# Optimization experiments

Hardware: AMD Instinct MI355X
Metric: run time of the kernel (lower is better)

## Reference

```python
import jax, jax.numpy as jnp
import numpy as np

D_MODEL = 768
N_HEADS = 12
D_HEAD = 64
N_MEM = 3072
ALPHA = 0.1
EPS = 1e-5
W_SCALE = 0.02  # standard init scale so energies/grads stay well-conditioned


def setup_inputs() -> dict:
    key = jax.random.key(0)
    k0, k1, k2, k3 = jax.random.split(key, 4)
    B, S = 8, 1024
    x = jax.random.normal(k0, (B, S, D_MODEL), jnp.float32)
    gamma = jnp.ones((1,), jnp.float32)                      # scalar LN gamma (ET uses a single gamma)
    delta = jnp.zeros((D_MODEL,), jnp.float32)               # LN bias
    Wq = jax.random.normal(k1, (N_HEADS, D_HEAD, D_MODEL), jnp.float32) * W_SCALE
    Wk = jax.random.normal(k2, (N_HEADS, D_HEAD, D_MODEL), jnp.float32) * W_SCALE
    beta = jnp.ones((N_HEADS,), jnp.float32) / np.sqrt(D_HEAD)  # per-head beta init 1/sqrt(d_head)
    xi = jax.random.normal(k3, (N_MEM, D_MODEL), jnp.float32) * W_SCALE
    return {"x": x, "gamma": gamma, "delta": delta, "Wq": Wq, "Wk": Wk,
            "beta": beta, "xi": xi, "n_steps": 12}


def _total_energy(x, gamma, delta, Wq, Wk, beta, xi):
    # --- EnergyLayerNorm: g = dL/dx, E_ln = <x, g> - L ---
    mean = jnp.mean(x, axis=-1, keepdims=True)
    xm = x - mean
    var = jnp.mean(xm * xm, axis=-1, keepdims=True)
    std = jnp.sqrt(var + EPS)
    g = gamma * xm / std + delta                       # (B,S,D)
    L = jnp.sum(D_MODEL * gamma * std) + jnp.sum(delta * x)
    e_ln = jnp.sum(x * g) - L
    # --- EnergyAttention: E = -sum_{b,h,q} (1/beta_h) * logsumexp_k(beta_h * Q.K) ---
    q = jnp.einsum('bsd,hyd->bhsy', g, Wq)
    k = jnp.einsum('bsd,hyd->bhsy', g, Wk)
    A = jnp.einsum('bhqy,bhky->bhqk', q, k)            # (B,H,S,S)
    lse = jax.nn.logsumexp(beta[None, :, None, None] * A, axis=-1)  # (B,H,S)
    e_attn = -jnp.sum(lse / beta[None, :, None])
    # --- HopfieldNetwork: E = -1/2 sum relu(g @ xi^T)^2 ---
    h = jnp.einsum('bsd,md->bsm', g, xi)               # (B,S,M)
    e_hop = -0.5 * jnp.sum(jnp.square(jax.nn.relu(h)))
    return e_ln + e_attn + e_hop


def reference(x, gamma, delta, Wq, Wk, beta, xi, n_steps):
    grad_fn = jax.grad(_total_energy, argnums=0)

    def step(state, _):
        return state - ALPHA * grad_fn(state, gamma, delta, Wq, Wk, beta, xi), None

    final, _ = jax.lax.scan(step, x, None, length=n_steps)
    return final
```

## Files before the change

kernel.cpp:

```cpp
#include <hip/hip_runtime.h>
#include <hip/hip_bf16.h>
#include <stdint.h>

#define T_TOK 8192
#define DM    768
#define NH    12
#define DH    64
#define SEQ   1024
#define NBH   96
#define NMEM  3072
#define NUP   4608
#define ALPHA 0.1f
#define EPS   1e-5f
#define NSTEPS 12
#define PAD   72
#define SPLITK 4

typedef unsigned short us;
typedef __bf16 bf16x8 __attribute__((ext_vector_type(8)));
typedef float  f32x4  __attribute__((ext_vector_type(4)));

__device__ __forceinline__ us f2bf(float f) {
  uint32_t u = __builtin_bit_cast(uint32_t, f);
  u += 0x7fffu + ((u >> 16) & 1u);
  return (us)(u >> 16);
}

__device__ __forceinline__ f32x4 mfma16(bf16x8 a, bf16x8 b, f32x4 c) {
  return __builtin_amdgcn_mfma_f32_16x16x32_bf16(a, b, c, 0, 0, 0);
}

__device__ __forceinline__ void gld16(const void* g, void* l) {
  __builtin_amdgcn_global_load_lds(
      (const __attribute__((address_space(1))) void*)(uintptr_t)g,
      (__attribute__((address_space(3))) void*)(uint32_t)(uintptr_t)l,
      16, 0, 0);
}

__device__ __forceinline__ float block_sum(float v, float* sb, int tid) {
#pragma unroll
  for (int d = 32; d >= 1; d >>= 1) v += __shfl_xor(v, d);
  __syncthreads();
  if ((tid & 63) == 0) sb[tid >> 6] = v;
  __syncthreads();
  return sb[0] + sb[1] + sb[2] + sb[3];
}

__global__ __launch_bounds__(256) void pack_w(const float* __restrict__ Wq,
                                              const float* __restrict__ Wk,
                                              const float* __restrict__ xi,
                                              us* __restrict__ Wup, us* __restrict__ WdT) {
  int idx = blockIdx.x * 256 + threadIdx.x;
  if (idx >= NUP * DM) return;
  int r = idx / DM, d = idx - r * DM;
  float v = (r < 768) ? Wq[idx] : (r < 1536 ? Wk[idx - 768 * DM] : xi[idx - 1536 * DM]);
  us h = f2bf(v);
  Wup[idx] = h;
  WdT[(size_t)d * NUP + r] = h;
}

__global__ __launch_bounds__(256) void ln_fwd(const float* __restrict__ X,
                                              const float* __restrict__ gamma,
                                              const float* __restrict__ delta,
                                              us* __restrict__ g_bf,
                                              float* __restrict__ meanb, float* __restrict__ rstdb) {
  int t = blockIdx.x, tid = threadIdx.x;
  const float* x = X + (size_t)t * DM;
  __shared__ float sb[4];
  float v0 = x[tid], v1 = x[tid + 256], v2 = x[tid + 512];
  float mean = block_sum(v0 + v1 + v2, sb, tid) * (1.0f / DM);
  float d0 = v0 - mean, d1 = v1 - mean, d2 = v2 - mean;
  float var = block_sum(d0 * d0 + d1 * d1 + d2 * d2, sb, tid) * (1.0f / DM);
  float rstd = rsqrtf(var + EPS);
  float gm = gamma[0];
  us* go = g_bf + (size_t)t * DM;
  go[tid]       = f2bf(gm * d0 * rstd + delta[tid]);
  go[tid + 256] = f2bf(gm * d1 * rstd + delta[tid + 256]);
  go[tid + 512] = f2bf(gm * d2 * rstd + delta[tid + 512]);
  if (tid == 0) { meanb[t] = mean; rstdb[t] = rstd; }
}

template <int MODE>
__global__ __launch_bounds__(256, 3) void gemm_bt(const us* __restrict__ A, const us* __restrict__ B,
                                                  int Kstride, int kchunk, us* __restrict__ QKout,
                                                  us* __restrict__ Dout, float* __restrict__ Gout) {
  __shared__ us As[3 * 128 * 32];
  __shared__ us Bs[3 * 128 * 32];
  int tid = threadIdx.x;
  int w = tid >> 6, lane = tid & 63, lm = lane & 15, lq = lane >> 4;
  int wm = (w >> 1) * 64, wn = (w & 1) * 64;

  int nwg  = gridDim.x * gridDim.y;
  int id   = blockIdx.y * gridDim.x + blockIdx.x;
  int qq   = nwg >> 3, rr = nwg & 7;
  int xcd  = id & 7, rank = id >> 3;
  int nid  = (xcd < rr ? xcd * (qq + 1) : rr * (qq + 1) + (xcd - rr) * qq) + rank;
  int bm   = nid % gridDim.x, bn = nid / gridDim.x;
  int m0 = bm * 128, n0 = bn * 128;
  int kbeg = blockIdx.z * kchunk;
  int NT = kchunk >> 5;

  int sr  = tid >> 2;
  int k8s = (tid & 3) ^ ((tid >> 3) & 3);
  const us* pa = A + (size_t)(m0 + sr) * Kstride + kbeg + k8s * 8;
  const us* pb = B + (size_t)(n0 + sr) * Kstride + kbeg + k8s * 8;
  const size_t hstep = (size_t)64 * Kstride;
  us* dA0 = &As[tid * 8];
  us* dB0 = &Bs[tid * 8];

  int kx   = (lq ^ ((lm >> 1) & 3)) * 8;
  int aoff = (wm + lm) * 32 + kx;
  int boff = (wn + lm) * 32 + kx;
  const us* Ar = As + aoff;
  const us* Br = Bs + boff;

  f32x4 zero4 = {0.f, 0.f, 0.f, 0.f};
  f32x4 acc[4][4];
#pragma unroll
  for (int i = 0; i < 4; i++)
#pragma unroll
    for (int j = 0; j < 4; j++) acc[i][j] = zero4;

#define STAGE_A(S, T) { gld16(pa + (size_t)(T) * 32,         dA0 + (S) * 4096); \
                        gld16(pa + (size_t)(T) * 32 + hstep, dA0 + (S) * 4096 + 2048); }
#define STAGE_B(S, T) { gld16(pb + (size_t)(T) * 32,         dB0 + (S) * 4096); \
                        gld16(pb + (size_t)(T) * 32 + hstep, dB0 + (S) * 4096 + 2048); }

  STAGE_A(0, 0); STAGE_B(0, 0);
  STAGE_A(1, 1); STAGE_B(1, 1);
  asm volatile("s_waitcnt vmcnt(4)" ::: "memory");
  __builtin_amdgcn_s_barrier();

#define ITER(T, S) {                                                            \
    bf16x8 af_[4], bf_[4];                                                      \
    _Pragma("unroll") for (int x = 0; x < 4; x++)                               \
      af_[x] = *(const bf16x8*)(Ar + (S) * 4096 + x * 512);                     \
    _Pragma("unroll") for (int x = 0; x < 4; x++)                               \
      bf_[x] = *(const bf16x8*)(Br + (S) * 4096 + x * 512);                     \
    if ((T) + 2 < NT) { STAGE_A(((S) + 2) % 3, (T) + 2);                        \
                        STAGE_B(((S) + 2) % 3, (T) + 2); }                      \
    _Pragma("unroll") for (int mt = 0; mt < 4; mt++)                            \
      _Pragma("unroll") for (int nt = 0; nt < 4; nt++)                          \
        acc[mt][nt] = mfma16(af_[mt], bf_[nt], acc[mt][nt]);                    \
    asm volatile("s_waitcnt lgkmcnt(0)" ::: "memory");                          \
    if ((T) + 2 < NT)      { asm volatile("s_waitcnt vmcnt(4)" ::: "memory"); } \
    else if ((T) + 1 < NT) { asm volatile("s_waitcnt vmcnt(0)" ::: "memory"); } \
    __builtin_amdgcn_s_barrier();                                               \
  }

  for (int t = 0; t < NT; t += 3) {
    ITER(t,     0);
    ITER(t + 1, 1);
    ITER(t + 2, 2);
  }
#undef ITER
#undef STAGE_A
#undef STAGE_B

  if (MODE == 0 && n0 < 1536) {
#pragma unroll
    for (int mt = 0; mt < 4; mt++) {
      int row = m0 + wm + mt * 16 + lq * 4;
#pragma unroll
      for (int nt = 0; nt < 4; nt++) {
        int col = n0 + wn + nt * 16 + lm;
#pragma unroll
        for (int r = 0; r < 4; r++)
          QKout[(size_t)(row + r) * 1536 + col] = f2bf(acc[mt][nt][r]);
      }
    }
  } else if (MODE == 0) {
#pragma unroll
    for (int mt = 0; mt < 4; mt++) {
      int row = m0 + wm + mt * 16 + lq * 4;
#pragma unroll
      for (int nt = 0; nt < 4; nt++) {
        int col = n0 + wn + nt * 16 + lm;
#pragma unroll
        for (int r = 0; r < 4; r++)
          Dout[(size_t)(row + r) * NUP + col] = f2bf(fmaxf(acc[mt][nt][r], 0.f));
      }
    }
  } else {
    float* Gz = Gout + (size_t)blockIdx.z * T_TOK * DM;
#pragma unroll
    for (int mt = 0; mt < 4; mt++) {
      int row = m0 + wm + mt * 16 + lq * 4;
#pragma unroll
      for (int nt = 0; nt < 4; nt++) {
        int col = n0 + wn + nt * 16 + lm;
#pragma unroll
        for (int r = 0; r < 4; r++)
          Gz[(size_t)(row + r) * DM + col] = acc[mt][nt][r];
      }
    }
  }
}

__global__ __launch_bounds__(256) void transpose_qk(const us* __restrict__ QK,
                                                    us* __restrict__ Qt, us* __restrict__ Kt) {
  int bh = blockIdx.x, kt = blockIdx.y, which = blockIdx.z;
  int b = bh / NH, h = bh - b * NH;
  int tid = threadIdx.x;
  __shared__ us tile[64][72];
  int c0 = h * 64 + (which ? 768 : 0);
  us* dst = (which ? Kt : Qt) + (size_t)bh * 64 * 1024;
#pragma unroll
  for (int r = 0; r < 2; r++) {
    int key = r * 32 + (tid >> 3); int yb = (tid & 7) * 8;
    *(bf16x8*)&tile[key][yb] =
        *(const bf16x8*)&QK[(size_t)(b * SEQ + kt * 64 + key) * 1536 + c0 + yb];
  }
  __syncthreads();
#pragma unroll
  for (int r = 0; r < 2; r++) {
    int lin = r * 256 + tid; int y = lin >> 3; int kb = (lin & 7) * 8;
    __align__(16) us tmp[8];
#pragma unroll
    for (int j = 0; j < 8; j++) tmp[j] = tile[kb + j][y];
    *(bf16x8*)&dst[(size_t)y * 1024 + kt * 64 + kb] = *(bf16x8*)tmp;
  }
}

__global__ __launch_bounds__(256) void attn_fwd(const us* __restrict__ QK, const us* __restrict__ Ktg,
                                                const float* __restrict__ beta,
                                                us* __restrict__ Dbuf, float* __restrict__ lse) {
  __shared__ us Qs[64 * PAD];
  __shared__ us Ks[64 * PAD];
  __shared__ us Kts[64 * PAD];
  __shared__ us Ps[4 * 16 * PAD];
  int bh = blockIdx.x, qt = blockIdx.y;
  int b = bh / NH, h = bh - b * NH;
  int tid = threadIdx.x, w = tid >> 6, lane = tid & 63, lm = lane & 15, lq = lane >> 4;
  float betah = beta[h];
#pragma unroll
  for (int r = 0; r < 2; r++) {
    int row = r * 32 + (tid >> 3); int yb = (tid & 7) * 8;
    *(bf16x8*)&Qs[row * PAD + yb] =
        *(const bf16x8*)&QK[(size_t)(b * SEQ + qt * 64 + row) * 1536 + h * 64 + yb];
  }
  __syncthreads();
  bf16x8 aq0 = *(const bf16x8*)&Qs[(w * 16 + lm) * PAD + lq * 8];
  bf16x8 aq1 = *(const bf16x8*)&Qs[(w * 16 + lm) * PAD + 32 + lq * 8];
  f32x4 zero = {0.f, 0.f, 0.f, 0.f};
  f32x4 O[4] = {zero, zero, zero, zero};
  float lacc[4] = {0.f, 0.f, 0.f, 0.f};
  us* pw = &Ps[w * 16 * PAD];

  for (int kc = 0; kc < SEQ; kc += 64) {
    __syncthreads();
#pragma unroll
    for (int r = 0; r < 2; r++) {
      int row = r * 32 + (tid >> 3); int yb = (tid & 7) * 8;
      *(bf16x8*)&Ks[row * PAD + yb] =
          *(const bf16x8*)&QK[(size_t)(b * SEQ + kc + row) * 1536 + 768 + h * 64 + yb];
      int lin = r * 256 + tid; int y = lin >> 3; int kb = (lin & 7) * 8;
      *(bf16x8*)&Kts[y * PAD + kb] =
          *(const bf16x8*)&Ktg[(size_t)(bh * 64 + y) * 1024 + kc + kb];
    }
    __syncthreads();
#pragma unroll
    for (int kk = 0; kk < 4; kk++) {
      f32x4 s = mfma16(aq0, *(const bf16x8*)&Ks[(kk * 16 + lm) * PAD + lq * 8], zero);
      s = mfma16(aq1, *(const bf16x8*)&Ks[(kk * 16 + lm) * PAD + 32 + lq * 8], s);
#pragma unroll
      for (int r = 0; r < 4; r++) {
        float p = __expf(betah * s[r]);
        lacc[r] += p;
        pw[(lq * 4 + r) * PAD + kk * 16 + lm] = f2bf(p);
      }
    }
    bf16x8 pa0 = *(const bf16x8*)&pw[lm * PAD + lq * 8];
    bf16x8 pa1 = *(const bf16x8*)&pw[lm * PAD + 32 + lq * 8];
#pragma unroll
    for (int nt = 0; nt < 4; nt++) {
      O[nt] = mfma16(pa0, *(const bf16x8*)&Kts[(nt * 16 + lm) * PAD + lq * 8], O[nt]);
      O[nt] = mfma16(pa1, *(const bf16x8*)&Kts[(nt * 16 + lm) * PAD + 32 + lq * 8], O[nt]);
    }
  }
  float l[4];
#pragma unroll
  for (int r = 0; r < 4; r++) {
    float v = lacc[r];
    v += __shfl_xor(v, 1); v += __shfl_xor(v, 2);
    v += __shfl_xor(v, 4); v += __shfl_xor(v, 8);
    l[r] = v;
  }
  float inv[4];
#pragma unroll
  for (int r = 0; r < 4; r++) inv[r] = 1.f / l[r];
#pragma unroll
  for (int nt = 0; nt < 4; nt++)
#pragma unroll
    for (int r = 0; r < 4; r++) {
      int q = qt * 64 + w * 16 + lq * 4 + r;
      Dbuf[(size_t)(b * SEQ + q) * NUP + h * 64 + nt * 16 + lm] = f2bf(O[nt][r] * inv[r]);
    }
  if (lm == 0) {
#pragma unroll
    for (int r = 0; r < 4; r++)
      lse[bh * SEQ + qt * 64 + w * 16 + lq * 4 + r] = __logf(l[r]);
  }
}

__global__ __launch_bounds__(256) void attn_bwd(const us* __restrict__ QK, const us* __restrict__ Qtg,
                                                const float* __restrict__ lse,
                                                const float* __restrict__ beta,
                                                us* __restrict__ Dbuf) {
  __shared__ us Ks2[64 * PAD];
  __shared__ us Qs2[64 * PAD];
  __shared__ us Qts[64 * PAD];
  __shared__ us Ps[4 * 16 * PAD];
  int bh = blockIdx.x, kt = blockIdx.y;
  int b = bh / NH, h = bh - b * NH;
  int tid = threadIdx.x, w = tid >> 6, lane = tid & 63, lm = lane & 15, lq = lane >> 4;
  float betah = beta[h];
#pragma unroll
  for (int r = 0; r < 2; r++) {
    int row = r * 32 + (tid >> 3); int yb = (tid & 7) * 8;
    *(bf16x8*)&Ks2[row * PAD + yb] =
        *(const bf16x8*)&QK[(size_t)(b * SEQ + kt * 64 + row) * 1536 + 768 + h * 64 + yb];
  }
  __syncthreads();
  bf16x8 ak0 = *(const bf16x8*)&Ks2[(w * 16 + lm) * PAD + lq * 8];
  bf16x8 ak1 = *(const bf16x8*)&Ks2[(w * 16 + lm) * PAD + 32 + lq * 8];
  f32x4 zero = {0.f, 0.f, 0.f, 0.f};
  f32x4 O[4] = {zero, zero, zero, zero};
  us* pw = &Ps[w * 16 * PAD];

  for (int qc = 0; qc < SEQ; qc += 64) {
    __syncthreads();
#pragma unroll
    for (int r = 0; r < 2; r++) {
      int row = r * 32 + (tid >> 3); int yb = (tid & 7) * 8;
      *(bf16x8*)&Qs2[row * PAD + yb] =
          *(const bf16x8*)&QK[(size_t)(b * SEQ + qc + row) * 1536 + h * 64 + yb];
      int lin = r * 256 + tid; int y = lin >> 3; int qb = (lin & 7) * 8;
      *(bf16x8*)&Qts[y * PAD + qb] =
          *(const bf16x8*)&Qtg[(size_t)(bh * 64 + y) * 1024 + qc + qb];
    }
    __syncthreads();
#pragma unroll
    for (int kk = 0; kk < 4; kk++) {
      f32x4 s = mfma16(ak0, *(const bf16x8*)&Qs2[(kk * 16 + lm) * PAD + lq * 8], zero);
      s = mfma16(ak1, *(const bf16x8*)&Qs2[(kk * 16 + lm) * PAD + 32 + lq * 8], s);
      float lv = lse[bh * SEQ + qc + kk * 16 + lm];
#pragma unroll
      for (int r = 0; r < 4; r++)
        pw[(lq * 4 + r) * PAD + kk * 16 + lm] = f2bf(__expf(betah * s[r] - lv));
    }
    bf16x8 pa0 = *(const bf16x8*)&pw[lm * PAD + lq * 8];
    bf16x8 pa1 = *(const bf16x8*)&pw[lm * PAD + 32 + lq * 8];
#pragma unroll
    for (int nt = 0; nt < 4; nt++) {
      O[nt] = mfma16(pa0, *(const bf16x8*)&Qts[(nt * 16 + lm) * PAD + lq * 8], O[nt]);
      O[nt] = mfma16(pa1, *(const bf16x8*)&Qts[(nt * 16 + lm) * PAD + 32 + lq * 8], O[nt]);
    }
  }
#pragma unroll
  for (int nt = 0; nt < 4; nt++)
#pragma unroll
    for (int r = 0; r < 4; r++) {
      int key = kt * 64 + w * 16 + lq * 4 + r;
      Dbuf[(size_t)(b * SEQ + key) * NUP + 768 + h * 64 + nt * 16 + lm] = f2bf(O[nt][r]);
    }
}

__global__ __launch_bounds__(256) void update_x(float* __restrict__ X, const float* __restrict__ G,
                                                float* __restrict__ meanb,
                                                float* __restrict__ rstdb,
                                                const float* __restrict__ gamma,
                                                const float* __restrict__ delta,
                                                us* __restrict__ g_bf) {
  int t = blockIdx.x, tid = threadIdx.x;
  __shared__ float sb[4];
  float mean = meanb[t], rstd = rstdb[t], gm = gamma[0];
  float* x = X + (size_t)t * DM;
  const float* g0 = G + (size_t)t * DM;
  const size_t GS = (size_t)T_TOK * DM;
  int i0 = tid, i1 = tid + 256, i2 = tid + 512;
  float x0 = x[i0], x1 = x[i1], x2 = x[i2];
  float gv0 = 0.f, gv1 = 0.f, gv2 = 0.f;
#pragma unroll
  for (int z = 0; z < SPLITK; z++) {
    gv0 += g0[i0 + z * GS];
    gv1 += g0[i1 + z * GS];
    gv2 += g0[i2 + z * GS];
  }
  float v0 = x0 - gv0, v1 = x1 - gv1, v2 = x2 - gv2;
  float n0 = (x0 - mean) * rstd, n1 = (x1 - mean) * rstd, n2 = (x2 - mean) * rstd;
  float s1 = block_sum(v0 + v1 + v2, sb, tid) * (1.0f / DM);
  float s2 = block_sum(v0 * n0 + v1 * n1 + v2 * n2, sb, tid) * (1.0f / DM);
  float c = ALPHA * gm * rstd;
  float y0 = x0 - c * (v0 - s1 - n0 * s2);
  float y1 = x1 - c * (v1 - s1 - n1 * s2);
  float y2 = x2 - c * (v2 - s1 - n2 * s2);
  x[i0] = y0; x[i1] = y1; x[i2] = y2;
  float mean2 = block_sum(y0 + y1 + y2, sb, tid) * (1.0f / DM);
  float d0 = y0 - mean2, d1 = y1 - mean2, d2 = y2 - mean2;
  float var2 = block_sum(d0 * d0 + d1 * d1 + d2 * d2, sb, tid) * (1.0f / DM);
  float rstd2 = rsqrtf(var2 + EPS);
  us* go = g_bf + (size_t)t * DM;
  go[i0] = f2bf(gm * d0 * rstd2 + delta[i0]);
  go[i1] = f2bf(gm * d1 * rstd2 + delta[i1]);
  go[i2] = f2bf(gm * d2 * rstd2 + delta[i2]);
  if (tid == 0) { meanb[t] = mean2; rstdb[t] = rstd2; }
}

extern "C" void kernel_launch(void* const* d_in, const int* in_sizes, int n_in,
                              void* d_out, int out_size, void* d_ws, size_t ws_size,
                              hipStream_t stream) {
  const float* x_in  = (const float*)d_in[0];
  const float* gamma = (const float*)d_in[1];
  const float* delta = (const float*)d_in[2];
  const float* Wq    = (const float*)d_in[3];
  const float* Wk    = (const float*)d_in[4];
  const float* beta  = (const float*)d_in[5];
  const float* xi    = (const float*)d_in[6];
  float* X = (float*)d_out;

  char* p = (char*)d_ws;
  auto carve = [&](size_t bytes) -> char* {
    char* q = p; p += (bytes + 255) & ~(size_t)255; return q;
  };
  us*    g_bf  = (us*)carve((size_t)T_TOK * DM * 2);
  float* meanb = (float*)carve((size_t)T_TOK * 4);
  float* rstdb = (float*)carve((size_t)T_TOK * 4);
  us*    QK    = (us*)carve((size_t)T_TOK * 1536 * 2);
  float* G     = (float*)carve((size_t)SPLITK * T_TOK * DM * 4);
  us*    Qt    = (us*)G;
  us*    Kt    = Qt + (size_t)NBH * 64 * 1024;
  float* lseb  = (float*)carve((size_t)NBH * SEQ * 4);
  us*    Dbuf  = (us*)carve((size_t)T_TOK * NUP * 2);
  us*    Wup   = (us*)carve((size_t)NUP * DM * 2);
  us*    WdT   = (us*)carve((size_t)DM * NUP * 2);

  hipMemcpyAsync(X, x_in, (size_t)T_TOK * DM * 4, hipMemcpyDeviceToDevice, stream);
  pack_w<<<(NUP * DM + 255) / 256, 256, 0, stream>>>(Wq, Wk, xi, Wup, WdT);
  ln_fwd<<<T_TOK, 256, 0, stream>>>(X, gamma, delta, g_bf, meanb, rstdb);

  for (int s = 0; s < NSTEPS; s++) {
    gemm_bt<0><<<dim3(64, 36, 1), 256, 0, stream>>>(g_bf, Wup, DM, DM, QK, Dbuf, nullptr);
    transpose_qk<<<dim3(NBH, 16, 2), 256, 0, stream>>>(QK, Qt, Kt);
    attn_fwd<<<dim3(NBH, 16), 256, 0, stream>>>(QK, Kt, beta, Dbuf, lseb);
    attn_bwd<<<dim3(NBH, 16), 256, 0, stream>>>(QK, Qt, lseb, beta, Dbuf);
    gemm_bt<1><<<dim3(64, 6, SPLITK), 256, 0, stream>>>(Dbuf, WdT, NUP, NUP / SPLITK,
                                                        nullptr, nullptr, G);
    update_x<<<T_TOK, 256, 0, stream>>>(X, G, meanb, rstdb, gamma, delta, g_bf);
  }
}
```

Measured before the change: 3.880 ms.

## Double-buffer LDS fragments in registers and deepen GEMM prefetch to three stages

The bf16 MFMA GEMM main loop now loads the next k-tile's LDS fragments into a second register set while the current tile's MFMAs run, using ping-pong register buffers. Global-to-LDS prefetch runs three tiles ahead instead of two, and the loop is unrolled by six to match. The goal is to hide LDS read latency and global load latency behind MFMA work. The cost is more VGPRs per thread, which could hurt occupancy under the 3-block launch bound, and it requires the k-tile count to be a multiple of six. Separately, MODE 1 tile rasterization is changed to walk the N dimension first, to improve cache reuse.

```diff
diff --git a/kernel.cpp b/kernel.cpp
--- a/kernel.cpp
+++ b/kernel.cpp
@@ -95,7 +95,9 @@
   int qq   = nwg >> 3, rr = nwg & 7;
   int xcd  = id & 7, rank = id >> 3;
   int nid  = (xcd < rr ? xcd * (qq + 1) : rr * (qq + 1) + (xcd - rr) * qq) + rank;
-  int bm   = nid % gridDim.x, bn = nid / gridDim.x;
+  int bm, bn;
+  if (MODE == 1) { bn = nid % gridDim.y; bm = nid / gridDim.y; }
+  else           { bm = nid % gridDim.x; bn = nid / gridDim.x; }
   int m0 = bm * 128, n0 = bn * 128;
   int kbeg = blockIdx.z * kchunk;
   int NT = kchunk >> 5;
@@ -121,6 +123,8 @@
 #pragma unroll
     for (int j = 0; j < 4; j++) acc[i][j] = zero4;
 
+  bf16x8 fa0[4], fb0[4], fa1[4], fb1[4];
+
 #define STAGE_A(S, T) { gld16(pa + (size_t)(T) * 32,         dA0 + (S) * 4096); \
                         gld16(pa + (size_t)(T) * 32 + hstep, dA0 + (S) * 4096 + 2048); }
 #define STAGE_B(S, T) { gld16(pb + (size_t)(T) * 32,         dB0 + (S) * 4096); \
@@ -128,30 +132,41 @@
 
   STAGE_A(0, 0); STAGE_B(0, 0);
   STAGE_A(1, 1); STAGE_B(1, 1);
+  STAGE_A(2, 2); STAGE_B(2, 2);
   asm volatile("s_waitcnt vmcnt(4)" ::: "memory");
   __builtin_amdgcn_s_barrier();
-
-#define ITER(T, S) {                                                            \
-    bf16x8 af_[4], bf_[4];                                                      \
-    _Pragma("unroll") for (int x = 0; x < 4; x++)                               \
-      af_[x] = *(const bf16x8*)(Ar + (S) * 4096 + x * 512);                     \
-    _Pragma("unroll") for (int x = 0; x < 4; x++)                               \
-      bf_[x] = *(const bf16x8*)(Br + (S) * 4096 + x * 512);                     \
-    if ((T) + 2 < NT) { STAGE_A(((S) + 2) % 3, (T) + 2);                        \
-                        STAGE_B(((S) + 2) % 3, (T) + 2); }                      \
+#pragma unroll
+  for (int x = 0; x < 4; x++) {
+    fa0[x] = *(const bf16x8*)(Ar + x * 512);
+    fb0[x] = *(const bf16x8*)(Br + x * 512);
+  }
+  asm volatile("s_waitcnt lgkmcnt(0)" ::: "memory");
+  __builtin_amdgcn_s_barrier();
+
+#define ITER(T, S, AC, BC, AN, BN2) {                                           \
+    if ((T) + 1 < NT) {                                                         \
+      _Pragma("unroll") for (int x = 0; x < 4; x++) {                           \
+        AN[x]  = *(const bf16x8*)(Ar + (((S) + 1) % 3) * 4096 + x * 512);       \
+        BN2[x] = *(const bf16x8*)(Br + (((S) + 1) % 3) * 4096 + x * 512);       \
+      }                                                                         \
+    }                                                                           \
+    if ((T) + 3 < NT) { STAGE_A(S, (T) + 3); STAGE_B(S, (T) + 3); }             \
     _Pragma("unroll") for (int mt = 0; mt < 4; mt++)                            \
       _Pragma("unroll") for (int nt = 0; nt < 4; nt++)                          \
-        acc[mt][nt] = mfma16(af_[mt], bf_[nt], acc[mt][nt]);                    \
+        acc[mt][nt] = mfma16(AC[mt], BC[nt], acc[mt][nt]);                      \
     asm volatile("s_waitcnt lgkmcnt(0)" ::: "memory");                          \
-    if ((T) + 2 < NT)      { asm volatile("s_waitcnt vmcnt(4)" ::: "memory"); } \
-    else if ((T) + 1 < NT) { asm volatile("s_waitcnt vmcnt(0)" ::: "memory"); } \
+    if ((T) + 3 < NT)      { asm volatile("s_waitcnt vmcnt(4)" ::: "memory"); } \
+    else if ((T) + 2 < NT) { asm volatile("s_waitcnt vmcnt(0)" ::: "memory"); } \
     __builtin_amdgcn_s_barrier();                                               \
   }
 
-  for (int t = 0; t < NT; t += 3) {
-    ITER(t,     0);
-    ITER(t + 1, 1);
-    ITER(t + 2, 2);
+  for (int t = 0; t < NT; t += 6) {
+    ITER(t,     0, fa0, fb0, fa1, fb1);
+    ITER(t + 1, 1, fa1, fb1, fa0, fb0);
+    ITER(t + 2, 2, fa0, fb0, fa1, fb1);
+    ITER(t + 3, 0, fa1, fb1, fa0, fb0);
+    ITER(t + 4, 1, fa0, fb0, fa1, fb1);
+    ITER(t + 5, 2, fa1, fb1, fa0, fb0);
   }
 #undef ITER
 #undef STAGE_A
```

Measured after the change: 5.279 ms. 1.36x slower.

## Switch GEMM to double-buffered LDS, swap MFMA operands for vector stores, drop XCD remap

Applied to the files above, without the earlier changes.

Reduces the GEMM's LDS pipeline from three stages to two, issuing the next tile's loads at the top of each iteration and waiting with vmcnt(0) before the barrier. Occupancy is raised to 4 waves per SIMD. MFMA operands are swapped so each lane holds four consecutive columns, which allows packed 8-byte bf16 and 16-byte fp32 vector stores instead of scalar ones. The XCD-aware block remapping is removed in favour of direct blockIdx tiling. The trade-off is less prefetch depth and possibly worse L2 locality across XCDs, in exchange for higher occupancy and cheaper epilogue stores.

```diff
diff --git a/kernel.cpp b/kernel.cpp
--- a/kernel.cpp
+++ b/kernel.cpp
@@ -81,22 +81,16 @@
 }
 
 template <int MODE>
-__global__ __launch_bounds__(256, 3) void gemm_bt(const us* __restrict__ A, const us* __restrict__ B,
+__global__ __launch_bounds__(256, 4) void gemm_bt(const us* __restrict__ A, const us* __restrict__ B,
                                                   int Kstride, int kchunk, us* __restrict__ QKout,
                                                   us* __restrict__ Dout, float* __restrict__ Gout) {
-  __shared__ us As[3 * 128 * 32];
-  __shared__ us Bs[3 * 128 * 32];
+  __shared__ us As[2 * 128 * 32];
+  __shared__ us Bs[2 * 128 * 32];
   int tid = threadIdx.x;
   int w = tid >> 6, lane = tid & 63, lm = lane & 15, lq = lane >> 4;
   int wm = (w >> 1) * 64, wn = (w & 1) * 64;
 
-  int nwg  = gridDim.x * gridDim.y;
-  int id   = blockIdx.y * gridDim.x + blockIdx.x;
-  int qq   = nwg >> 3, rr = nwg & 7;
-  int xcd  = id & 7, rank = id >> 3;
-  int nid  = (xcd < rr ? xcd * (qq + 1) : rr * (qq + 1) + (xcd - rr) * qq) + rank;
-  int bm   = nid % gridDim.x, bn = nid / gridDim.x;
-  int m0 = bm * 128, n0 = bn * 128;
+  int m0 = blockIdx.x * 128, n0 = blockIdx.y * 128;
   int kbeg = blockIdx.z * kchunk;
   int NT = kchunk >> 5;
 
@@ -108,11 +102,9 @@
   us* dA0 = &As[tid * 8];
   us* dB0 = &Bs[tid * 8];
 
-  int kx   = (lq ^ ((lm >> 1) & 3)) * 8;
-  int aoff = (wm + lm) * 32 + kx;
-  int boff = (wn + lm) * 32 + kx;
-  const us* Ar = As + aoff;
-  const us* Br = Bs + boff;
+  int kx = (lq ^ ((lm >> 1) & 3)) * 8;
+  const us* Ar = As + (wm + lm) * 32 + kx;
+  const us* Br = Bs + (wn + lm) * 32 + kx;
 
   f32x4 zero4 = {0.f, 0.f, 0.f, 0.f};
   f32x4 acc[4][4];
@@ -121,78 +113,74 @@
 #pragma unroll
     for (int j = 0; j < 4; j++) acc[i][j] = zero4;
 
-#define STAGE_A(S, T) { gld16(pa + (size_t)(T) * 32,         dA0 + (S) * 4096); \
-                        gld16(pa + (size_t)(T) * 32 + hstep, dA0 + (S) * 4096 + 2048); }
-#define STAGE_B(S, T) { gld16(pb + (size_t)(T) * 32,         dB0 + (S) * 4096); \
-                        gld16(pb + (size_t)(T) * 32 + hstep, dB0 + (S) * 4096 + 2048); }
-
-  STAGE_A(0, 0); STAGE_B(0, 0);
-  STAGE_A(1, 1); STAGE_B(1, 1);
-  asm volatile("s_waitcnt vmcnt(4)" ::: "memory");
+#define STAGE(S, T) { gld16(pa + (size_t)(T) * 32,         dA0 + (S) * 4096);        \
+                      gld16(pa + (size_t)(T) * 32 + hstep, dA0 + (S) * 4096 + 2048); \
+                      gld16(pb + (size_t)(T) * 32,         dB0 + (S) * 4096);        \
+                      gld16(pb + (size_t)(T) * 32 + hstep, dB0 + (S) * 4096 + 2048); }
+
+  STAGE(0, 0);
+  asm volatile("s_waitcnt vmcnt(0)" ::: "memory");
   __builtin_amdgcn_s_barrier();
 
 #define ITER(T, S) {                                                            \
+    if ((T) + 1 < NT) STAGE((S) ^ 1, (T) + 1);                                  \
     bf16x8 af_[4], bf_[4];                                                      \
     _Pragma("unroll") for (int x = 0; x < 4; x++)                               \
       af_[x] = *(const bf16x8*)(Ar + (S) * 4096 + x * 512);                     \
     _Pragma("unroll") for (int x = 0; x < 4; x++)                               \
       bf_[x] = *(const bf16x8*)(Br + (S) * 4096 + x * 512);                     \
-    if ((T) + 2 < NT) { STAGE_A(((S) + 2) % 3, (T) + 2);                        \
-                        STAGE_B(((S) + 2) % 3, (T) + 2); }                      \
     _Pragma("unroll") for (int mt = 0; mt < 4; mt++)                            \
       _Pragma("unroll") for (int nt = 0; nt < 4; nt++)                          \
-        acc[mt][nt] = mfma16(af_[mt], bf_[nt], acc[mt][nt]);                    \
-    asm volatile("s_waitcnt lgkmcnt(0)" ::: "memory");                          \
-    if ((T) + 2 < NT)      { asm volatile("s_waitcnt vmcnt(4)" ::: "memory"); } \
-    else if ((T) + 1 < NT) { asm volatile("s_waitcnt vmcnt(0)" ::: "memory"); } \
-    __builtin_amdgcn_s_barrier();                                               \
-  }
-
-  for (int t = 0; t < NT; t += 3) {
+        acc[mt][nt] = mfma16(bf_[nt], af_[mt], acc[mt][nt]);       \
+    if ((T) + 1 < NT) {                                                         \
+      asm volatile("s_waitcnt lgkmcnt(0)" ::: "memory");                        \
+      asm volatile("s_waitcnt vmcnt(0)" ::: "memory");                          \
+      __builtin_amdgcn_s_barrier();                                             \
+    }                                                                           \
+  }
+
+  for (int t = 0; t < NT; t += 2) {
     ITER(t,     0);
     ITER(t + 1, 1);
-    ITER(t + 2, 2);
   }
 #undef ITER
-#undef STAGE_A
-#undef STAGE_B
-
+#undef STAGE
+
+  int cb = wn + lq * 4;
   if (MODE == 0 && n0 < 1536) {
 #pragma unroll
     for (int mt = 0; mt < 4; mt++) {
-      int row = m0 + wm + mt * 16 + lq * 4;
+      us* rowp = QKout + (size_t)(m0 + wm + mt * 16 + lm) * 1536 + n0 + cb;
 #pragma unroll
       for (int nt = 0; nt < 4; nt++) {
-        int col = n0 + wn + nt * 16 + lm;
-#pragma unroll
-        for (int r = 0; r < 4; r++)
-          QKout[(size_t)(row + r) * 1536 + col] = f2bf(acc[mt][nt][r]);
+        f32x4 v = acc[mt][nt];
+        uint2 p;
+        p.x = (uint32_t)f2bf(v[0]) | ((uint32_t)f2bf(v[1]) << 16);
+        p.y = (uint32_t)f2bf(v[2]) | ((uint32_t)f2bf(v[3]) << 16);
+        *(uint2*)(rowp + nt * 16) = p;
       }
     }
   } else if (MODE == 0) {
 #pragma unroll
     for (int mt = 0; mt < 4; mt++) {
-      int row = m0 + wm + mt * 16 + lq * 4;
+      us* rowp = Dout + (size_t)(m0 + wm + mt * 16 + lm) * NUP + n0 + cb;
 #pragma unroll
       for (int nt = 0; nt < 4; nt++) {
-        int col = n0 + wn + nt * 16 + lm;
-#pragma unroll
-        for (int r = 0; r < 4; r++)
-          Dout[(size_t)(row + r) * NUP + col] = f2bf(fmaxf(acc[mt][nt][r], 0.f));
+        f32x4 v = acc[mt][nt];
+        uint2 p;
+        p.x = (uint32_t)f2bf(fmaxf(v[0], 0.f)) | ((uint32_t)f2bf(fmaxf(v[1], 0.f)) << 16);
+        p.y = (uint32_t)f2bf(fmaxf(v[2], 0.f)) | ((uint32_t)f2bf(fmaxf(v[3], 0.f)) << 16);
+        *(uint2*)(rowp + nt * 16) = p;
       }
     }
   } else {
     float* Gz = Gout + (size_t)blockIdx.z * T_TOK * DM;
 #pragma unroll
     for (int mt = 0; mt < 4; mt++) {
-      int row = m0 + wm + mt * 16 + lq * 4;
-#pragma unroll
-      for (int nt = 0; nt < 4; nt++) {
-        int col = n0 + wn + nt * 16 + lm;
-#pragma unroll
-        for (int r = 0; r < 4; r++)
-          Gz[(size_t)(row + r) * DM + col] = acc[mt][nt][r];
-      }
+      float* rowp = Gz + (size_t)(m0 + wm + mt * 16 + lm) * DM + n0 + cb;
+#pragma unroll
+      for (int nt = 0; nt < 4; nt++)
+        *(f32x4*)(rowp + nt * 16) = acc[mt][nt];
     }
   }
 }
```

Measured after the change: 3.605 ms. 1.08x faster.
